# Optimization experiments

Measured on AMD Instinct MI355X. Metric: run time of the kernel, lower is better.

The kernel has to match this reference:

```python
import jax, jax.numpy as jnp
import numpy as np

N_NODES = 20000   # len(pert2id)
N_EDGES = 400000  # top_20 graph: ~20 edges/node
BATCH   = 4096
IN_DIM  = 64
HID_DIM = 128
OUT_DIM = 64
HEADS   = 2
HEAD_D  = HID_DIM // HEADS  # 64 (also OUT_DIM per head on last layer)


def setup_inputs() -> dict:
    key = jax.random.key(0)
    ks = jax.random.split(key, 24)
    inp = {
        "pert_indices": jax.random.randint(ks[0], (BATCH,), 0, N_NODES),
        "edge_index": jax.random.randint(ks[1], (2, N_EDGES), 0, N_NODES),
        "edge_weight": jax.random.uniform(ks[2], (N_EDGES,), dtype=jnp.float32),
        "emb": jax.random.normal(ks[3], (N_NODES, IN_DIM), dtype=jnp.float32) * 0.02,
    }
    # 4 GATv2 layers: layer0 IN->HEADS*HEAD_D (concat), layers 1,2 HID->HEADS*HEAD_D (concat),
    # layer3 HID->HEADS*OUT_DIM (mean over heads -> OUT_DIM)
    in_dims = [IN_DIM, HID_DIM, HID_DIM, HID_DIM]
    concat = [True, True, True, False]
    k = 4
    for i in range(4):
        d_in = in_dims[i]
        d_head = HEAD_D
        sc = 1.0 / np.sqrt(d_in)
        inp[f"Wl{i}"] = jax.random.normal(ks[k], (d_in, HEADS * d_head), dtype=jnp.float32) * sc; k += 1
        inp[f"Wr{i}"] = jax.random.normal(ks[k], (d_in, HEADS * d_head), dtype=jnp.float32) * sc; k += 1
        inp[f"a{i}"]  = jax.random.normal(ks[k], (HEADS, d_head), dtype=jnp.float32) * (1.0 / np.sqrt(d_head)); k += 1
        out_dim = HEADS * d_head if concat[i] else d_head
        inp[f"b{i}"]  = jnp.zeros((out_dim,), dtype=jnp.float32); k += 1
    return inp


def _gatv2_layer(x, src, dst, ew, Wl, Wr, a, b, concat):
    N = x.shape[0]
    H, D = a.shape
    xl = (x @ Wl).reshape(N, H, D)   # source transform (messages)
    xr = (x @ Wr).reshape(N, H, D)   # target transform
    # GATv2 score: a^T LeakyReLU(Wl x_j + Wr x_i) per edge, per head -> [E, H]
    e = jnp.einsum("ehd,hd->eh", jax.nn.leaky_relu(xl[src] + xr[dst], 0.2), a)
    # segment softmax over incoming edges of each target node
    m = jax.ops.segment_max(e, dst, num_segments=N)
    m = jnp.where(jnp.isfinite(m), m, 0.0)  # isolated nodes
    ex = jnp.exp(e - m[dst])
    s = jax.ops.segment_sum(ex, dst, num_segments=N)
    alpha = ex / (s[dst] + 1e-16)            # [E, H]
    msg = (alpha * ew[:, None])[:, :, None] * xl[src]  # edge-weighted messages [E,H,D]
    out = jax.ops.segment_sum(msg, dst, num_segments=N)  # [N,H,D]
    out = out.reshape(N, H * D) if concat else out.mean(axis=1)
    return out + b


def reference(pert_indices, edge_index, edge_weight, emb,
              Wl0, Wr0, a0, b0, Wl1, Wr1, a1, b1,
              Wl2, Wr2, a2, b2, Wl3, Wr3, a3, b3):
    src, dst = edge_index[0], edge_index[1]
    layers = [(Wl0, Wr0, a0, b0, True), (Wl1, Wr1, a1, b1, True),
              (Wl2, Wr2, a2, b2, True), (Wl3, Wr3, a3, b3, False)]
    x = emb
    for i, (Wl, Wr, a, b, cc) in enumerate(layers):
        x = _gatv2_layer(x, src, dst, edge_weight, Wl, Wr, a, b, cc)
        if i < len(layers) - 1:
            x = jax.nn.elu(x)
    # node_emb[pert_indices]
    return x[pert_indices]
```

## Files before the change

### kernel.cpp

```cpp
#include <hip/hip_runtime.h>
#include <hip/hip_fp16.h>
#include <math.h>

#define N_NODES 20000
#define N_EDGES 400000
#define BATCH   4096
#define MTILES  (N_NODES / 16)
#define XSCALE  1024.0f
#define XINV    (1.0f / 1024.0f)

typedef __attribute__((ext_vector_type(8))) short short8v;
typedef __attribute__((ext_vector_type(4))) float f32x4;
typedef __attribute__((ext_vector_type(2))) _Float16 h2v;

__device__ __forceinline__ float fdot2h(h2v a, h2v b, float c)
{
#if __has_builtin(__builtin_amdgcn_fdot2)
    return __builtin_amdgcn_fdot2(a, b, c, false);
#else
    return fmaf((float)a[0], (float)b[0], fmaf((float)a[1], (float)b[1], c));
#endif
}

__device__ __forceinline__ h2v mk_h2(float x, float y)
{
    h2v r; r[0] = (_Float16)x; r[1] = (_Float16)y; return r;
}

__device__ __forceinline__ void bf16split(float v, short& h, short& l)
{
    unsigned u  = __float_as_uint(v);
    unsigned hu = u & 0xFFFF0000u;
    h = (short)(hu >> 16);
    const float lo = v - __uint_as_float(hu);
    l = (short)(__float_as_uint(lo) >> 16);
}

__global__ __launch_bounds__(256)
void prep_kernel(int* __restrict__ deg,
                 const float* __restrict__ Wl0, const float* __restrict__ Wr0,
                 const float* __restrict__ Wl1, const float* __restrict__ Wr1,
                 const float* __restrict__ Wl2, const float* __restrict__ Wr2,
                 const float* __restrict__ Wl3, const float* __restrict__ Wr3,
                 short* __restrict__ wpk)
{
    const int t = blockIdx.x * 256 + threadIdx.x;
    if (t < N_NODES) { deg[t] = 0; return; }
    const int tp = t - N_NODES;
    if (tp >= 14336) return;
    int layer, base, K;
    const float *Wl, *Wr;
    if (tp < 2048)       { layer = 0; base = 0;     K = 64;  Wl = Wl0; Wr = Wr0; }
    else if (tp < 6144)  { layer = 1; base = 2048;  K = 128; Wl = Wl1; Wr = Wr1; }
    else if (tp < 10240) { layer = 2; base = 6144;  K = 128; Wl = Wl2; Wr = Wr2; }
    else                 { layer = 3; base = 10240; K = 128; Wl = Wl3; Wr = Wr3; }
    const int KB   = K / 32;
    const int tt   = tp - base;
    const int lane = tt & 63;
    const int kb   = (tt >> 6) % KB;
    const int nt   = tt / (64 * KB);
    const float* W = (nt < 8) ? Wl : Wr;
    const int col  = (nt & 7) * 16 + (lane & 15);
    const int k0   = kb * 32 + (lane >> 4) * 8;
    short8v h, l;
#pragma unroll
    for (int e = 0; e < 8; ++e) {
        short hh, ll; bf16split(W[(size_t)(k0 + e) * 128 + col], hh, ll);
        h[e] = hh; l[e] = ll;
    }
    short* ob = wpk + (size_t)layer * 65536
                    + ((size_t)(nt * KB + kb) * 2) * 512 + lane * 8;
    *(short8v*)ob         = h;
    *(short8v*)(ob + 512) = l;
}

template<int KB, int NWAVES>
__global__ __launch_bounds__(NWAVES * 64)
void mfma_transform_kernel(const float* __restrict__ x,
                           const short* __restrict__ wpk,
                           __half* __restrict__ xlh, float* __restrict__ xr)
{
    constexpr int K  = KB * 32;
    constexpr int KP = K + 4;
    __shared__ float xs[16 * KP];
    const int mtile = blockIdx.x;
    const int wid   = threadIdx.x >> 6;
    const int lane  = threadIdx.x & 63;

    {
        const float4* __restrict__ src = (const float4*)(x + (size_t)mtile * 16 * K);
        for (int idx = threadIdx.x; idx < 16 * K / 4; idx += NWAVES * 64) {
            const int row = idx / (K / 4), c4 = idx % (K / 4);
            *(float4*)(xs + row * KP + c4 * 4) = src[idx];
        }
    }
    __syncthreads();

    short8v ah[KB], al[KB];
    {
        const float* ab = xs + (lane & 15) * KP + (lane >> 4) * 8;
#pragma unroll
        for (int kb = 0; kb < KB; ++kb) {
            const float4 f0 = *(const float4*)(ab + kb * 32);
            const float4 f1 = *(const float4*)(ab + kb * 32 + 4);
            float tmp[8] = {f0.x, f0.y, f0.z, f0.w, f1.x, f1.y, f1.z, f1.w};
#pragma unroll
            for (int e = 0; e < 8; ++e) {
                short hh, ll; bf16split(tmp[e], hh, ll);
                ah[kb][e] = hh; al[kb][e] = ll;
            }
        }
    }

#pragma unroll
    for (int i = 0; i < 4; ++i) {
        const int nt = wid * 4 + i;
        const short* bb = wpk + ((size_t)nt * KB * 2) * 512 + lane * 8;
        f32x4 acc = {0.f, 0.f, 0.f, 0.f};
#pragma unroll
        for (int kb = 0; kb < KB; ++kb) {
            const short8v bh = *(const short8v*)(bb + (size_t)(kb * 2 + 0) * 512);
            const short8v bl = *(const short8v*)(bb + (size_t)(kb * 2 + 1) * 512);
            acc = __builtin_amdgcn_mfma_f32_16x16x32_bf16(ah[kb], bh, acc, 0, 0, 0);
            acc = __builtin_amdgcn_mfma_f32_16x16x32_bf16(ah[kb], bl, acc, 0, 0, 0);
            acc = __builtin_amdgcn_mfma_f32_16x16x32_bf16(al[kb], bh, acc, 0, 0, 0);
        }
        const int colb = (nt & 7) * 16 + (lane & 15);
        const int row0 = mtile * 16 + (lane >> 4) * 4;
        if (nt < 8) {
#pragma unroll
            for (int r = 0; r < 4; ++r)
                xlh[(size_t)(row0 + r) * 128 + colb] = __float2half(acc[r] * XSCALE);
        } else {
#pragma unroll
            for (int r = 0; r < 4; ++r)
                xr[(size_t)(row0 + r) * 128 + colb] = acc[r];
        }
    }
}

__global__ __launch_bounds__(128)
void l3_fused_kernel(const float* __restrict__ x, const short* __restrict__ wpk,
                     __half* __restrict__ xlh,
                     const int* __restrict__ pert, const float* __restrict__ Wr3,
                     float* __restrict__ xr)
{
    constexpr int K  = 128;
    constexpr int KP = K + 4;
    __shared__ float xs[16 * KP];

    if (blockIdx.x < MTILES) {
        const int mtile = blockIdx.x;
        const int wid   = threadIdx.x >> 6;
        const int lane  = threadIdx.x & 63;
        {
            const float4* __restrict__ src = (const float4*)(x + (size_t)mtile * 16 * K);
            for (int idx = threadIdx.x; idx < 16 * K / 4; idx += 128) {
                const int row = idx / (K / 4), c4 = idx % (K / 4);
                *(float4*)(xs + row * KP + c4 * 4) = src[idx];
            }
        }
        __syncthreads();

        short8v ah[4], al[4];
        {
            const float* ab = xs + (lane & 15) * KP + (lane >> 4) * 8;
#pragma unroll
            for (int kb = 0; kb < 4; ++kb) {
                const float4 f0 = *(const float4*)(ab + kb * 32);
                const float4 f1 = *(const float4*)(ab + kb * 32 + 4);
                float tmp[8] = {f0.x, f0.y, f0.z, f0.w, f1.x, f1.y, f1.z, f1.w};
#pragma unroll
                for (int e = 0; e < 8; ++e) {
                    short hh, ll; bf16split(tmp[e], hh, ll);
                    ah[kb][e] = hh; al[kb][e] = ll;
                }
            }
        }
#pragma unroll
        for (int i = 0; i < 4; ++i) {
            const int nt = wid * 4 + i;
            const short* bb = wpk + ((size_t)nt * 4 * 2) * 512 + lane * 8;
            f32x4 acc = {0.f, 0.f, 0.f, 0.f};
#pragma unroll
            for (int kb = 0; kb < 4; ++kb) {
                const short8v bh = *(const short8v*)(bb + (size_t)(kb * 2 + 0) * 512);
                const short8v bl = *(const short8v*)(bb + (size_t)(kb * 2 + 1) * 512);
                acc = __builtin_amdgcn_mfma_f32_16x16x32_bf16(ah[kb], bh, acc, 0, 0, 0);
                acc = __builtin_amdgcn_mfma_f32_16x16x32_bf16(ah[kb], bl, acc, 0, 0, 0);
                acc = __builtin_amdgcn_mfma_f32_16x16x32_bf16(al[kb], bh, acc, 0, 0, 0);
            }
            const int colb = (nt & 7) * 16 + (lane & 15);
            const int row0 = mtile * 16 + (lane >> 4) * 4;
#pragma unroll
            for (int r = 0; r < 4; ++r)
                xlh[(size_t)(row0 + r) * 128 + colb] = __float2half(acc[r] * XSCALE);
        }
    } else {
        constexpr int G = 8;
        const int t  = threadIdx.x;
        const int i0 = (blockIdx.x - MTILES) * G;

        const float* __restrict__ xrow[G];
#pragma unroll
        for (int g = 0; g < G; ++g)
            xrow[g] = x + (size_t)pert[i0 + g] * K;

        float acc[G];
#pragma unroll
        for (int g = 0; g < G; ++g) acc[g] = 0.f;

        float4 xA[G], xB[G];
        float wA[4], wB[4];

        auto loadc = [&](float4* xv, float* w, int k) {
#pragma unroll
            for (int g = 0; g < G; ++g)
                xv[g] = *(const float4*)(xrow[g] + k);
#pragma unroll
            for (int u = 0; u < 4; ++u) w[u] = Wr3[(k + u) * 128 + t];
        };
        auto fmac = [&](const float4* xv, const float* w) {
#pragma unroll
            for (int g = 0; g < G; ++g) {
                acc[g] = fmaf(xv[g].x, w[0], acc[g]);
                acc[g] = fmaf(xv[g].y, w[1], acc[g]);
                acc[g] = fmaf(xv[g].z, w[2], acc[g]);
                acc[g] = fmaf(xv[g].w, w[3], acc[g]);
            }
        };

        loadc(xA, wA, 0);
        for (int k0 = 0; k0 < K; k0 += 8) {
            if (k0 + 4 < K) loadc(xB, wB, k0 + 4);
            fmac(xA, wA);
            if (k0 + 8 < K) loadc(xA, wA, k0 + 8);
            fmac(xB, wB);
        }
#pragma unroll
        for (int g = 0; g < G; ++g)
            xr[(size_t)(i0 + g) * 128 + t] = acc[g];
    }
}

__global__ __launch_bounds__(256)
void count_deg_kernel(const int* __restrict__ dst, int* __restrict__ deg, int E)
{
    const int e = blockIdx.x * blockDim.x + threadIdx.x;
    if (e < E) atomicAdd(&deg[dst[e]], 1);
}

#define CHUNK 20
#define SCAN_PAD (1024 * CHUNK)
__global__ __launch_bounds__(1024)
void scan_kernel(const int* __restrict__ deg, int* __restrict__ off,
                 int* __restrict__ cursor)
{
    __shared__ int xs[SCAN_PAD];
    __shared__ int sums[1024];
    const int t = threadIdx.x;
    for (int i = t; i < SCAN_PAD; i += 1024)
        xs[i] = (i < N_NODES) ? deg[i] : 0;
    __syncthreads();

    const int base = t * CHUNK;
    int local[CHUNK];
    int s = 0;
#pragma unroll
    for (int i = 0; i < CHUNK; ++i) {
        local[i] = s;
        s += xs[base + i];
    }
    sums[t] = s;
    __syncthreads();
    for (int d = 1; d < 1024; d <<= 1) {
        int v = (t >= d) ? sums[t - d] : 0;
        __syncthreads();
        sums[t] += v;
        __syncthreads();
    }
    const int prev = (t == 0) ? 0 : sums[t - 1];
#pragma unroll
    for (int i = 0; i < CHUNK; ++i)
        xs[base + i] = prev + local[i];
    __syncthreads();
    for (int i = t; i < N_NODES; i += 1024) {
        const int o = xs[i];
        off[i] = o;
        cursor[i] = o;
    }
    if (t == 1023) off[N_NODES] = sums[1023];
}

__global__ __launch_bounds__(256)
void scatter_kernel(const int* __restrict__ src, const int* __restrict__ dst,
                    const float* __restrict__ ew, int* __restrict__ cursor,
                    int* __restrict__ ssrc, float* __restrict__ sew, int E)
{
    const int e = blockIdx.x * blockDim.x + threadIdx.x;
    if (e >= E) return;
    const int p = atomicAdd(&cursor[dst[e]], 1);
    ssrc[p] = src[e];
    sew[p]  = ew[e];
}

template<int LAST>
__global__ __launch_bounds__(256)
void gat_node_kernel(const __half* __restrict__ xl, const float* __restrict__ xr,
                     const int* __restrict__ off, const int* __restrict__ ssrc,
                     const float* __restrict__ sew, const float* __restrict__ a,
                     const float* __restrict__ b, float* __restrict__ xout,
                     const int* __restrict__ nodemap, int nnodes)
{
    const int widx = (int)((blockIdx.x * blockDim.x + threadIdx.x) >> 6);
    if (widx >= nnodes) return;
    const int node = LAST ? nodemap[widx] : widx;
    const int xrrow = widx;
    const int lane = threadIdx.x & 63;
    const int q  = lane >> 4;
    const int h  = (lane >> 3) & 1;
    const int j  = lane & 7;
    const int cb = h * 64 + j * 8;

    const float* xrp = xr + (size_t)xrrow * 128 + cb;
    const h2v r01 = mk_h2(xrp[0] * XSCALE, xrp[1] * XSCALE);
    const h2v r23 = mk_h2(xrp[2] * XSCALE, xrp[3] * XSCALE);
    const h2v r45 = mk_h2(xrp[4] * XSCALE, xrp[5] * XSCALE);
    const h2v r67 = mk_h2(xrp[6] * XSCALE, xrp[7] * XSCALE);
    const h2v a01 = mk_h2(a[cb],     a[cb + 1]);
    const h2v a23 = mk_h2(a[cb + 2], a[cb + 3]);
    const h2v a45 = mk_h2(a[cb + 4], a[cb + 5]);
    const h2v a67 = mk_h2(a[cb + 6], a[cb + 7]);

    const int e0 = off[node], e1 = off[node + 1];
    const int nr = (e1 - e0 + 3) >> 2;

    float m = -1e30f, s = 0.f;
    float4 accA = {0,0,0,0}, accB = {0,0,0,0};

    auto lde = [&](int r, float& w, bool& valid, uint4& raw) {
        const int ei  = e0 + r * 4 + q;
        valid = ei < e1;
        const int eic = valid ? ei : (e1 - 1);
        const int sn  = ssrc[eic];
        w = valid ? sew[eic] : 0.f;
        raw = *(const uint4*)(xl + (size_t)sn * 128 + cb);
    };
    auto plrelu = [](h2v v) {
        return __builtin_elementwise_max(v, v * (_Float16)0.2f);
    };

    float w_c; bool v_c; uint4 raw_c;
    if (nr > 0) lde(0, w_c, v_c, raw_c);

    for (int r = 0; r < nr; ++r) {
        float w_n; bool v_n; uint4 raw_n;
        if (r + 1 < nr) lde(r + 1, w_n, v_n, raw_n);

        const h2v x01 = __builtin_bit_cast(h2v, raw_c.x);
        const h2v x23 = __builtin_bit_cast(h2v, raw_c.y);
        const h2v x45 = __builtin_bit_cast(h2v, raw_c.z);
        const h2v x67 = __builtin_bit_cast(h2v, raw_c.w);

        const h2v v01 = plrelu(x01 + r01);
        const h2v v23 = plrelu(x23 + r23);
        const h2v v45 = plrelu(x45 + r45);
        const h2v v67 = plrelu(x67 + r67);
        float p = fdot2h(v01, a01, 0.f);
        p = fdot2h(v23, a23, p);
        p = fdot2h(v45, a45, p);
        p = fdot2h(v67, a67, p);
        p += __shfl_xor(p, 1, 64);
        p += __shfl_xor(p, 2, 64);
        p += __shfl_xor(p, 4, 64);
        p = v_c ? p * XINV : -1e30f;

        const float f0x = (float)x01[0], f0y = (float)x01[1];
        const float f1x = (float)x23[0], f1y = (float)x23[1];
        const float f2x = (float)x45[0], f2y = (float)x45[1];
        const float f3x = (float)x67[0], f3y = (float)x67[1];

        const float d = p - m;
        if (__any(d > 8.f)) {
            const float t   = __expf(-fabsf(d));
            const bool  pos = d > 0.f;
            const float rr  = pos ? t : 1.f;
            const float ex  = pos ? 1.f : t;
            m = pos ? p : m;
            const float c = ex * w_c;
            s = s * rr + ex;
            accA.x = fmaf(c, f0x, accA.x * rr); accA.y = fmaf(c, f0y, accA.y * rr);
            accA.z = fmaf(c, f1x, accA.z * rr); accA.w = fmaf(c, f1y, accA.w * rr);
            accB.x = fmaf(c, f2x, accB.x * rr); accB.y = fmaf(c, f2y, accB.y * rr);
            accB.z = fmaf(c, f3x, accB.z * rr); accB.w = fmaf(c, f3y, accB.w * rr);
        } else {
            const float ex = __expf(d);
            const float c  = ex * w_c;
            s += ex;
            accA.x = fmaf(c, f0x, accA.x); accA.y = fmaf(c, f0y, accA.y);
            accA.z = fmaf(c, f1x, accA.z); accA.w = fmaf(c, f1y, accA.w);
            accB.x = fmaf(c, f2x, accB.x); accB.y = fmaf(c, f2y, accB.y);
            accB.z = fmaf(c, f3x, accB.z); accB.w = fmaf(c, f3y, accB.w);
        }

        w_c = w_n; v_c = v_n; raw_c = raw_n;
    }

    float mg = fmaxf(m, __shfl_xor(m, 16, 64));
    mg = fmaxf(mg, __shfl_xor(mg, 32, 64));
    const float rq = __expf(m - mg);
    float sq = s * rq;
    sq += __shfl_xor(sq, 16, 64);
    sq += __shfl_xor(sq, 32, 64);
    auto redsum2 = [](float v) {
        v += __shfl_xor(v, 16, 64);
        return v + __shfl_xor(v, 32, 64);
    };
    accA.x = redsum2(accA.x * rq); accA.y = redsum2(accA.y * rq);
    accA.z = redsum2(accA.z * rq); accA.w = redsum2(accA.w * rq);
    accB.x = redsum2(accB.x * rq); accB.y = redsum2(accB.y * rq);
    accB.z = redsum2(accB.z * rq); accB.w = redsum2(accB.w * rq);
    const float inv = XINV / (sq + 1e-16f);

    if (!LAST) {
        if (q == 0) {
            const float4 bA = *(const float4*)(b + cb);
            const float4 bB = *(const float4*)(b + cb + 4);
            float4 oA, oB;
            oA.x = accA.x * inv + bA.x; oA.x = oA.x > 0.f ? oA.x : expm1f(oA.x);
            oA.y = accA.y * inv + bA.y; oA.y = oA.y > 0.f ? oA.y : expm1f(oA.y);
            oA.z = accA.z * inv + bA.z; oA.z = oA.z > 0.f ? oA.z : expm1f(oA.z);
            oA.w = accA.w * inv + bA.w; oA.w = oA.w > 0.f ? oA.w : expm1f(oA.w);
            oB.x = accB.x * inv + bB.x; oB.x = oB.x > 0.f ? oB.x : expm1f(oB.x);
            oB.y = accB.y * inv + bB.y; oB.y = oB.y > 0.f ? oB.y : expm1f(oB.y);
            oB.z = accB.z * inv + bB.z; oB.z = oB.z > 0.f ? oB.z : expm1f(oB.z);
            oB.w = accB.w * inv + bB.w; oB.w = oB.w > 0.f ? oB.w : expm1f(oB.w);
            float* op = xout + (size_t)node * 128;
            *(float4*)(op + cb)     = oA;
            *(float4*)(op + cb + 4) = oB;
        }
    } else {
        float oA[4] = {accA.x * inv, accA.y * inv, accA.z * inv, accA.w * inv};
        float oB[4] = {accB.x * inv, accB.y * inv, accB.z * inv, accB.w * inv};
        float pA[4], pB[4];
#pragma unroll
        for (int k = 0; k < 4; ++k) {
            pA[k] = __shfl_xor(oA[k], 8, 64);
            pB[k] = __shfl_xor(oB[k], 8, 64);
        }
        if (q == 0 && h == 0) {
            const float4 bA = *(const float4*)(b + j * 8);
            const float4 bB = *(const float4*)(b + j * 8 + 4);
            float* op = xout + (size_t)widx * 64 + j * 8;
            op[0] = 0.5f * (oA[0] + pA[0]) + bA.x;
            op[1] = 0.5f * (oA[1] + pA[1]) + bA.y;
            op[2] = 0.5f * (oA[2] + pA[2]) + bA.z;
            op[3] = 0.5f * (oA[3] + pA[3]) + bA.w;
            op[4] = 0.5f * (oB[0] + pB[0]) + bB.x;
            op[5] = 0.5f * (oB[1] + pB[1]) + bB.y;
            op[6] = 0.5f * (oB[2] + pB[2]) + bB.z;
            op[7] = 0.5f * (oB[3] + pB[3]) + bB.w;
        }
    }
}

extern "C" void kernel_launch(void* const* d_in, const int* in_sizes, int n_in,
                              void* d_out, int out_size, void* d_ws, size_t ws_size,
                              hipStream_t stream)
{
    const int*   pert = (const int*)d_in[0];
    const int*   eidx = (const int*)d_in[1];
    const float* ew   = (const float*)d_in[2];
    const float* emb  = (const float*)d_in[3];
    const float* Wl[4] = {(const float*)d_in[4],  (const float*)d_in[8],
                          (const float*)d_in[12], (const float*)d_in[16]};
    const float* Wr[4] = {(const float*)d_in[5],  (const float*)d_in[9],
                          (const float*)d_in[13], (const float*)d_in[17]};
    const float* av[4] = {(const float*)d_in[6],  (const float*)d_in[10],
                          (const float*)d_in[14], (const float*)d_in[18]};
    const float* bv[4] = {(const float*)d_in[7],  (const float*)d_in[11],
                          (const float*)d_in[15], (const float*)d_in[19]};

    const int N = N_NODES, E = N_EDGES;
    const int* srcp = eidx;
    const int* dstp = eidx + E;

    float*  ws   = (float*)d_ws;
    float*  xbuf = ws;
    __half* xlh  = (__half*)(xbuf + (size_t)N * 128);
    float*  xr   = (float*)(xlh + (size_t)N * 128);
    short*  wpk  = (short*)(xr + (size_t)N * 128);
    int*    deg  = (int*)(wpk + 4 * 65536);
    int*    off  = deg + N;
    int*    cur  = off + N + 1;
    int*    ssrc = cur + N;
    float*  sew  = (float*)(ssrc + E);

    prep_kernel<<<(N + 14336 + 255) / 256, 256, 0, stream>>>(
        deg, Wl[0], Wr[0], Wl[1], Wr[1], Wl[2], Wr[2], Wl[3], Wr[3], wpk);
    count_deg_kernel<<<(E + 255) / 256, 256, 0, stream>>>(dstp, deg, E);
    scan_kernel<<<1, 1024, 0, stream>>>(deg, off, cur);
    scatter_kernel<<<(E + 255) / 256, 256, 0, stream>>>(srcp, dstp, ew, cur,
                                                        ssrc, sew, E);

    mfma_transform_kernel<2, 4><<<MTILES, 256, 0, stream>>>(emb, wpk, xlh, xr);
    gat_node_kernel<0><<<(N * 64 + 255) / 256, 256, 0, stream>>>(
        xlh, xr, off, ssrc, sew, av[0], bv[0], xbuf, nullptr, N);

    for (int layer = 1; layer < 3; ++layer) {
        mfma_transform_kernel<4, 4><<<MTILES, 256, 0, stream>>>(
            xbuf, wpk + layer * 65536, xlh, xr);
        gat_node_kernel<0><<<(N * 64 + 255) / 256, 256, 0, stream>>>(
            xlh, xr, off, ssrc, sew, av[layer], bv[layer], xbuf, nullptr, N);
    }

    l3_fused_kernel<<<MTILES + BATCH / 8, 128, 0, stream>>>(
        xbuf, wpk + 3 * 65536, xlh, pert, Wr[3], xr);
    gat_node_kernel<1><<<(BATCH * 64 + 255) / 256, 256, 0, stream>>>(
        xlh, xr, off, ssrc, sew, av[3], bv[3], (float*)d_out, pert, BATCH);
}
```

Before: 222.0 us.

## Emit MFMA-ready bf16 split fragments from GAT epilogue to skip transform staging

The node aggregation kernel now writes its ELU output as pre-split bf16 hi/lo operands already laid out in MFMA A-fragment order. The next layer's transform (and the layer-3 fused kernel) loads these fragments directly, so it no longer stages fp32 rows through shared memory or redoes the bf16 split. The fp32 activation buffer is written only where still needed (layer 2, for the Wr3 gather path). This removes shared-memory staging and conversion work from the transform kernels. In exchange the aggregation epilogue does the split and issues scattered 16-byte fragment stores.

New measurement: 229.6 us. 1.03x slower.

```diff
diff --git a/kernel.cpp b/kernel.cpp
--- a/kernel.cpp
+++ b/kernel.cpp
@@ -139,43 +139,67 @@
     }
 }
 
+__global__ __launch_bounds__(256)
+void mfma_transform_frag_kernel(const short* __restrict__ xfrag,
+                                const short* __restrict__ wpk,
+                                __half* __restrict__ xlh, float* __restrict__ xr)
+{
+    const int mtile = blockIdx.x;
+    const int wid   = threadIdx.x >> 6;
+    const int lane  = threadIdx.x & 63;
+
+    short8v ah[4], al[4];
+    const short* ab = xfrag + ((size_t)mtile * 4 * 2) * 512 + lane * 8;
+#pragma unroll
+    for (int kb = 0; kb < 4; ++kb) {
+        ah[kb] = *(const short8v*)(ab + (size_t)(kb * 2 + 0) * 512);
+        al[kb] = *(const short8v*)(ab + (size_t)(kb * 2 + 1) * 512);
+    }
+
+#pragma unroll
+    for (int i = 0; i < 4; ++i) {
+        const int nt = wid * 4 + i;
+        const short* bb = wpk + ((size_t)nt * 4 * 2) * 512 + lane * 8;
+        f32x4 acc = {0.f, 0.f, 0.f, 0.f};
+#pragma unroll
+        for (int kb = 0; kb < 4; ++kb) {
+            const short8v bh = *(const short8v*)(bb + (size_t)(kb * 2 + 0) * 512);
+            const short8v bl = *(const short8v*)(bb + (size_t)(kb * 2 + 1) * 512);
+            acc = __builtin_amdgcn_mfma_f32_16x16x32_bf16(ah[kb], bh, acc, 0, 0, 0);
+            acc = __builtin_amdgcn_mfma_f32_16x16x32_bf16(ah[kb], bl, acc, 0, 0, 0);
+            acc = __builtin_amdgcn_mfma_f32_16x16x32_bf16(al[kb], bh, acc, 0, 0, 0);
+        }
+        const int colb = (nt & 7) * 16 + (lane & 15);
+        const int row0 = mtile * 16 + (lane >> 4) * 4;
+        if (nt < 8) {
+#pragma unroll
+            for (int r = 0; r < 4; ++r)
+                xlh[(size_t)(row0 + r) * 128 + colb] = __float2half(acc[r] * XSCALE);
+        } else {
+#pragma unroll
+            for (int r = 0; r < 4; ++r)
+                xr[(size_t)(row0 + r) * 128 + colb] = acc[r];
+        }
+    }
+}
+
 __global__ __launch_bounds__(128)
-void l3_fused_kernel(const float* __restrict__ x, const short* __restrict__ wpk,
-                     __half* __restrict__ xlh,
+void l3_fused_kernel(const short* __restrict__ xfrag, const float* __restrict__ x,
+                     const short* __restrict__ wpk, __half* __restrict__ xlh,
                      const int* __restrict__ pert, const float* __restrict__ Wr3,
                      float* __restrict__ xr)
 {
-    constexpr int K  = 128;
-    constexpr int KP = K + 4;
-    __shared__ float xs[16 * KP];
-
     if (blockIdx.x < MTILES) {
         const int mtile = blockIdx.x;
         const int wid   = threadIdx.x >> 6;
         const int lane  = threadIdx.x & 63;
-        {
-            const float4* __restrict__ src = (const float4*)(x + (size_t)mtile * 16 * K);
-            for (int idx = threadIdx.x; idx < 16 * K / 4; idx += 128) {
-                const int row = idx / (K / 4), c4 = idx % (K / 4);
-                *(float4*)(xs + row * KP + c4 * 4) = src[idx];
-            }
-        }
-        __syncthreads();
 
         short8v ah[4], al[4];
-        {
-            const float* ab = xs + (lane & 15) * KP + (lane >> 4) * 8;
-#pragma unroll
-            for (int kb = 0; kb < 4; ++kb) {
-                const float4 f0 = *(const float4*)(ab + kb * 32);
-                const float4 f1 = *(const float4*)(ab + kb * 32 + 4);
-                float tmp[8] = {f0.x, f0.y, f0.z, f0.w, f1.x, f1.y, f1.z, f1.w};
-#pragma unroll
-                for (int e = 0; e < 8; ++e) {
-                    short hh, ll; bf16split(tmp[e], hh, ll);
-                    ah[kb][e] = hh; al[kb][e] = ll;
-                }
-            }
+        const short* ab = xfrag + ((size_t)mtile * 4 * 2) * 512 + lane * 8;
+#pragma unroll
+        for (int kb = 0; kb < 4; ++kb) {
+            ah[kb] = *(const short8v*)(ab + (size_t)(kb * 2 + 0) * 512);
+            al[kb] = *(const short8v*)(ab + (size_t)(kb * 2 + 1) * 512);
         }
 #pragma unroll
         for (int i = 0; i < 4; ++i) {
@@ -198,6 +222,7 @@
         }
     } else {
         constexpr int G = 8;
+        constexpr int K = 128;
         const int t  = threadIdx.x;
         const int i0 = (blockIdx.x - MTILES) * G;
 
@@ -304,17 +329,18 @@
     sew[p]  = ew[e];
 }
 
-template<int LAST>
+template<int MODE>
 __global__ __launch_bounds__(256)
 void gat_node_kernel(const __half* __restrict__ xl, const float* __restrict__ xr,
                      const int* __restrict__ off, const int* __restrict__ ssrc,
                      const float* __restrict__ sew, const float* __restrict__ a,
                      const float* __restrict__ b, float* __restrict__ xout,
+                     short* __restrict__ xfrag,
                      const int* __restrict__ nodemap, int nnodes)
 {
     const int widx = (int)((blockIdx.x * blockDim.x + threadIdx.x) >> 6);
     if (widx >= nnodes) return;
-    const int node = LAST ? nodemap[widx] : widx;
+    const int node = (MODE == 2) ? nodemap[widx] : widx;
     const int xrrow = widx;
     const int lane = threadIdx.x & 63;
     const int q  = lane >> 4;
@@ -422,22 +448,38 @@
     accB.z = redsum2(accB.z * rq); accB.w = redsum2(accB.w * rq);
     const float inv = XINV / (sq + 1e-16f);
 
-    if (!LAST) {
+    if (MODE < 2) {
         if (q == 0) {
             const float4 bA = *(const float4*)(b + cb);
             const float4 bB = *(const float4*)(b + cb + 4);
-            float4 oA, oB;
-            oA.x = accA.x * inv + bA.x; oA.x = oA.x > 0.f ? oA.x : expm1f(oA.x);
-            oA.y = accA.y * inv + bA.y; oA.y = oA.y > 0.f ? oA.y : expm1f(oA.y);
-            oA.z = accA.z * inv + bA.z; oA.z = oA.z > 0.f ? oA.z : expm1f(oA.z);
-            oA.w = accA.w * inv + bA.w; oA.w = oA.w > 0.f ? oA.w : expm1f(oA.w);
-            oB.x = accB.x * inv + bB.x; oB.x = oB.x > 0.f ? oB.x : expm1f(oB.x);
-            oB.y = accB.y * inv + bB.y; oB.y = oB.y > 0.f ? oB.y : expm1f(oB.y);
-            oB.z = accB.z * inv + bB.z; oB.z = oB.z > 0.f ? oB.z : expm1f(oB.z);
-            oB.w = accB.w * inv + bB.w; oB.w = oB.w > 0.f ? oB.w : expm1f(oB.w);
-            float* op = xout + (size_t)node * 128;
-            *(float4*)(op + cb)     = oA;
-            *(float4*)(op + cb + 4) = oB;
+            float ov[8];
+            ov[0] = accA.x * inv + bA.x; ov[0] = ov[0] > 0.f ? ov[0] : expm1f(ov[0]);
+            ov[1] = accA.y * inv + bA.y; ov[1] = ov[1] > 0.f ? ov[1] : expm1f(ov[1]);
+            ov[2] = accA.z * inv + bA.z; ov[2] = ov[2] > 0.f ? ov[2] : expm1f(ov[2]);
+            ov[3] = accA.w * inv + bA.w; ov[3] = ov[3] > 0.f ? ov[3] : expm1f(ov[3]);
+            ov[4] = accB.x * inv + bB.x; ov[4] = ov[4] > 0.f ? ov[4] : expm1f(ov[4]);
+            ov[5] = accB.y * inv + bB.y; ov[5] = ov[5] > 0.f ? ov[5] : expm1f(ov[5]);
+            ov[6] = accB.z * inv + bB.z; ov[6] = ov[6] > 0.f ? ov[6] : expm1f(ov[6]);
+            ov[7] = accB.w * inv + bB.w; ov[7] = ov[7] > 0.f ? ov[7] : expm1f(ov[7]);
+
+            const int mtile = node >> 4;
+            const int kb    = cb >> 5;
+            const int fl    = (node & 15) + ((j & 3) << 4);
+            short8v hi8, lo8;
+#pragma unroll
+            for (int e = 0; e < 8; ++e) {
+                short hh, ll; bf16split(ov[e], hh, ll);
+                hi8[e] = hh; lo8[e] = ll;
+            }
+            short* fb = xfrag + ((size_t)(mtile * 4 + kb) * 2) * 512 + fl * 8;
+            *(short8v*)fb         = hi8;
+            *(short8v*)(fb + 512) = lo8;
+
+            if (MODE == 1) {
+                float* op = xout + (size_t)node * 128;
+                *(float4*)(op + cb)     = make_float4(ov[0], ov[1], ov[2], ov[3]);
+                *(float4*)(op + cb + 4) = make_float4(ov[4], ov[5], ov[6], ov[7]);
+            }
         }
     } else {
         float oA[4] = {accA.x * inv, accA.y * inv, accA.z * inv, accA.w * inv};
@@ -490,7 +532,8 @@
     __half* xlh  = (__half*)(xbuf + (size_t)N * 128);
     float*  xr   = (float*)(xlh + (size_t)N * 128);
     short*  wpk  = (short*)(xr + (size_t)N * 128);
-    int*    deg  = (int*)(wpk + 4 * 65536);
+    short*  xfrag= wpk + 4 * 65536;
+    int*    deg  = (int*)(xfrag + (size_t)MTILES * 4 * 2 * 512);
     int*    off  = deg + N;
     int*    cur  = off + N + 1;
     int*    ssrc = cur + N;
@@ -505,17 +548,20 @@
 
     mfma_transform_kernel<2, 4><<<MTILES, 256, 0, stream>>>(emb, wpk, xlh, xr);
     gat_node_kernel<0><<<(N * 64 + 255) / 256, 256, 0, stream>>>(
-        xlh, xr, off, ssrc, sew, av[0], bv[0], xbuf, nullptr, N);
-
-    for (int layer = 1; layer < 3; ++layer) {
-        mfma_transform_kernel<4, 4><<<MTILES, 256, 0, stream>>>(
-            xbuf, wpk + layer * 65536, xlh, xr);
-        gat_node_kernel<0><<<(N * 64 + 255) / 256, 256, 0, stream>>>(
-            xlh, xr, off, ssrc, sew, av[layer], bv[layer], xbuf, nullptr, N);
-    }
+        xlh, xr, off, ssrc, sew, av[0], bv[0], xbuf, xfrag, nullptr, N);
+
+    mfma_transform_frag_kernel<<<MTILES, 256, 0, stream>>>(
+        xfrag, wpk + 1 * 65536, xlh, xr);
+    gat_node_kernel<0><<<(N * 64 + 255) / 256, 256, 0, stream>>>(
+        xlh, xr, off, ssrc, sew, av[1], bv[1], xbuf, xfrag, nullptr, N);
+
+    mfma_transform_frag_kernel<<<MTILES, 256, 0, stream>>>(
+        xfrag, wpk + 2 * 65536, xlh, xr);
+    gat_node_kernel<1><<<(N * 64 + 255) / 256, 256, 0, stream>>>(
+        xlh, xr, off, ssrc, sew, av[2], bv[2], xbuf, xfrag, nullptr, N);
 
     l3_fused_kernel<<<MTILES + BATCH / 8, 128, 0, stream>>>(
-        xbuf, wpk + 3 * 65536, xlh, pert, Wr[3], xr);
-    gat_node_kernel<1><<<(BATCH * 64 + 255) / 256, 256, 0, stream>>>(
-        xlh, xr, off, ssrc, sew, av[3], bv[3], (float*)d_out, pert, BATCH);
-}
+        xfrag, xbuf, wpk + 3 * 65536, xlh, pert, Wr[3], xr);
+    gat_node_kernel<2><<<(BATCH * 64 + 255) / 256, 256, 0, stream>>>(
+        xlh, xr, off, ssrc, sew, av[3], bv[3], (float*)d_out, xfrag, pert, BATCH);
+}
```
